# Optimization experiments

Measured on AMD Instinct MI355X. Metric: run time of the kernel, lower is better.

## Reference

```python
import jax, jax.numpy as jnp
import numpy as np

BATCH = 8192
EMBED = 1024
NFEAT = 32768
TOPK = 64


def setup_inputs() -> dict:
    key = jax.random.key(0)
    k1, k2, k3 = jax.random.split(key, 3)
    embed = jax.random.normal(k1, (BATCH, EMBED), dtype=jnp.float32)
    # nn.Linear-style init scale
    enc_w = jax.random.normal(k2, (NFEAT, EMBED), dtype=jnp.float32) * (1.0 / np.sqrt(EMBED))
    enc_b = jnp.zeros((NFEAT,), dtype=jnp.float32)
    dec_table = jax.random.normal(k3, (NFEAT, EMBED), dtype=jnp.float32)
    return {"embed": embed, "enc_w": enc_w, "enc_b": enc_b, "dec_table": dec_table}


def reference(embed, enc_w, enc_b, dec_table):
    # Encoder: linear + sigmoid -> [B, NFEAT]
    project = jax.nn.sigmoid(jnp.einsum('be,fe->bf', embed, enc_w) + enc_b)
    # Top-k selection along feature dim
    weights, feats = jax.lax.top_k(project, TOPK)   # [B, K] each
    # Decoder: gather embeddings and weighted sum -> [B, EMBED]
    vecs = dec_table[feats]                          # [B, K, EMBED]
    return jnp.einsum('bk,bke->be', weights, vecs)
```

## Files before the change

kernel.cpp:

```cpp
#include <hip/hip_runtime.h>
#include <hip/hip_bf16.h>

#define BATCH 8192
#define EMBED 1024
#define NFEAT 32768
#define TOPK  64
#define NT    16

#define CAP  512
#define GCAP 768
#define AMB  128
#define EPS2 0.028f
#define TMUL 2.4f

typedef __attribute__((ext_vector_type(8))) short bf16x8;
typedef __attribute__((ext_vector_type(4))) float f32x4;
typedef unsigned long long u64;

__device__ __forceinline__ void gload_lds16(const void* g, void* l) {
  __builtin_amdgcn_global_load_lds(
      (const __attribute__((address_space(1))) unsigned int*)g,
      (__attribute__((address_space(3))) unsigned int*)l, 16, 0, 0);
}

__device__ __forceinline__ unsigned short f2bf(float f) {
  unsigned int u = __float_as_uint(f);
  u += 0x7fffu + ((u >> 16) & 1u);
  return (unsigned short)(u >> 16);
}
__device__ __forceinline__ float bf2f(unsigned short u) {
  return __uint_as_float(((unsigned int)u) << 16);
}

__global__ __launch_bounds__(256) void k_zero(int* __restrict__ p, int n) {
  int i = blockIdx.x * 256 + threadIdx.x;
  if (i < n) p[i] = 0;
}

__global__ __launch_bounds__(256) void k_cvt(const float* __restrict__ in,
                                             unsigned short* __restrict__ out, long n) {
  long i = ((long)blockIdx.x * blockDim.x + threadIdx.x) * 4;
  long stride = (long)gridDim.x * blockDim.x * 4;
  for (; i < n; i += stride) {
    f32x4 v = *(const f32x4*)(in + i);
    u64 pk = (u64)f2bf(v[0]) | ((u64)f2bf(v[1]) << 16) |
             ((u64)f2bf(v[2]) << 32) | ((u64)f2bf(v[3]) << 48);
    *(u64*)(out + i) = pk;
  }
}

__global__ __launch_bounds__(256) void k_norm(const float* __restrict__ embed,
                                              float* __restrict__ T0) {
  const int row = blockIdx.x * 4 + (threadIdx.x >> 6);
  const int lane = threadIdx.x & 63;
  const float* e = embed + (size_t)row * EMBED;
  float ss = 0.f;
  for (int j = lane * 4; j < EMBED; j += 256) {
    f32x4 v = *(const f32x4*)(e + j);
    ss += v[0]*v[0] + v[1]*v[1] + v[2]*v[2] + v[3]*v[3];
  }
  #pragma unroll
  for (int off = 32; off > 0; off >>= 1) ss += __shfl_down(ss, off);
  if (lane == 0) T0[row] = TMUL * sqrtf(ss) * (1.0f / 32.0f);
}

#define PHASE(BUF, MH, NH, STG)                                               \
  {                                                                           \
    if (NH == 0) {                                                            \
      _Pragma("unroll")                                                       \
      for (int mi = 0; mi < 4; ++mi) {                                        \
        const int ar = wr * 128 + MH * 64 + mi * 16 + l15;                    \
        a[mi][0] = *(const bf16x8*)&As[BUF][ar][k0];                          \
        a[mi][1] = *(const bf16x8*)&As[BUF][ar][k1];                          \
      }                                                                       \
    }                                                                         \
    if (MH == 0) {                                                            \
      _Pragma("unroll")                                                       \
      for (int ni = 0; ni < 2; ++ni) {                                        \
        const int br = wc * 64 + NH * 32 + ni * 16 + l15;                     \
        (NH ? b1 : b0)[ni][0] = *(const bf16x8*)&Bs[BUF][br][k0];             \
        (NH ? b1 : b0)[ni][1] = *(const bf16x8*)&Bs[BUF][br][k1];             \
      }                                                                       \
    }                                                                         \
    STG;                                                                      \
    asm volatile("s_waitcnt vmcnt(8)" ::: "memory");                          \
    __builtin_amdgcn_s_barrier();                                             \
    __builtin_amdgcn_s_setprio(1);                                            \
    _Pragma("unroll")                                                         \
    for (int mi = 0; mi < 4; ++mi) {                                          \
      _Pragma("unroll")                                                       \
      for (int ni = 0; ni < 2; ++ni) {                                        \
        acc[MH*4+mi][NH*2+ni] = __builtin_amdgcn_mfma_f32_16x16x32_bf16(      \
            a[mi][0], (NH ? b1 : b0)[ni][0], acc[MH*4+mi][NH*2+ni], 0, 0, 0); \
        acc[MH*4+mi][NH*2+ni] = __builtin_amdgcn_mfma_f32_16x16x32_bf16(      \
            a[mi][1], (NH ? b1 : b0)[ni][1], acc[MH*4+mi][NH*2+ni], 0, 0, 0); \
      }                                                                       \
    }                                                                         \
    __builtin_amdgcn_s_setprio(0);                                            \
    __builtin_amdgcn_s_barrier();                                             \
  }

__global__ __launch_bounds__(512, 2) void k_gemm(
    const unsigned short* __restrict__ A,
    const unsigned short* __restrict__ B,
    const float* __restrict__ bias,
    const float* __restrict__ T0,
    u64* __restrict__ gent,
    int* __restrict__ cntB)
{
  __shared__ unsigned short As[2][256][64];
  __shared__ unsigned short Bs[2][256][64];
  __shared__ float T0s[256];
  __shared__ float lval[GCAP];
  __shared__ int   lpak[GCAP];
  __shared__ int   lcnt;

  const int tid = threadIdx.x;
  const int w = tid >> 6, lane = tid & 63;
  const int l15 = lane & 15, l4 = lane >> 4;
  const int wr = w >> 2, wc = w & 3;

  const int id = blockIdx.y * gridDim.x + blockIdx.x;
  const int xcd = id & 7;
  const int idx = id >> 3;
  const int ntile = xcd * 16 + (idx & 15);
  const int mtile = idx >> 4;

  const unsigned short* Ag = A + (size_t)mtile * 256 * EMBED;
  const unsigned short* Bg = B + (size_t)ntile * 256 * EMBED;

  const int rr = tid >> 3;
  const int u3 = tid & 7;
  const int scol = (u3 ^ (rr & 7)) << 3;
  const size_t aoff = (size_t)rr * EMBED + scol;
  const int brr = ((rr >> 5) << 6) + (rr & 31);
  const size_t boff = (size_t)brr * EMBED + scol;
  const int wrow = w * 8;
  const int bdst = ((w >> 2) << 6) + ((w & 3) << 3);

  const int k0 = (l4 ^ (l15 & 7)) << 3;
  const int k1 = k0 ^ 32;

  auto SA = [&](int tt, int r0, int r1) {
    if (tt < NT) {
      const int bb = tt & 1;
      const size_t kt = (size_t)tt * 64;
      gload_lds16(Ag + (size_t)r0 * EMBED + kt + aoff, (void*)&As[bb][r0 + wrow][0]);
      gload_lds16(Ag + (size_t)r1 * EMBED + kt + aoff, (void*)&As[bb][r1 + wrow][0]);
    }
  };
  auto SB = [&](int tt, int sb) {
    if (tt < NT) {
      const int bb = tt & 1;
      const size_t kt = (size_t)tt * 64;
      gload_lds16(Bg + (size_t)sb * EMBED + kt + boff, (void*)&Bs[bb][sb + bdst][0]);
      gload_lds16(Bg + (size_t)(sb + 128) * EMBED + kt + boff,
                  (void*)&Bs[bb][sb + 128 + bdst][0]);
    }
  };

  f32x4 acc[8][4] = {};
  bf16x8 a[4][2], b0[2][2], b1[2][2];

  SA(0, 0, 128); SB(0, 0); SB(0, 32); SA(0, 64, 192); SA(1, 0, 128); SB(1, 0);
  asm volatile("s_waitcnt vmcnt(8)" ::: "memory");
  __builtin_amdgcn_s_barrier();

  for (int t = 0; t < NT; t += 2) {
    PHASE(0, 0, 0, SB(t + 1, 32));
    PHASE(0, 0, 1, SA(t + 1, 64, 192));
    PHASE(0, 1, 0, SA(t + 2, 0, 128));
    PHASE(0, 1, 1, SB(t + 2, 0));
    PHASE(1, 0, 0, SB(t + 2, 32));
    PHASE(1, 0, 1, SA(t + 2, 64, 192));
    PHASE(1, 1, 0, SA(t + 3, 0, 128));
    PHASE(1, 1, 1, SB(t + 3, 0));
  }

  if (tid == 0) lcnt = 0;
  if (tid < 256) T0s[tid] = T0[mtile * 256 + tid];
  __syncthreads();

  const int col = l15, rg = l4 * 4;
  #pragma unroll
  for (int N = 0; N < 4; ++N) {
    const int n = ntile * 256 + wc * 64 + N * 16 + col;
    const float bv = bias[n];
    #pragma unroll
    for (int M = 0; M < 8; ++M) {
      const int rbase = wr * 128 + M * 16 + rg;
      #pragma unroll
      for (int j = 0; j < 4; ++j) {
        const float s = acc[M][N][j] + bv;
        const int rl = rbase + j;
        if (s >= T0s[rl]) {
          const int p = atomicAdd(&lcnt, 1);
          if (p < GCAP) { lval[p] = s; lpak[p] = (rl << 16) | n; }
        }
      }
    }
  }
  __syncthreads();
  const int bslot = mtile * 128 + ntile;
  int c = lcnt; if (c > GCAP) c = GCAP;
  if (tid == 0) cntB[bslot] = c;
  u64* gb = gent + (size_t)bslot * GCAP;
  for (int e = tid; e < c; e += 512)
    gb[e] = ((u64)(unsigned)lpak[e] << 32) | (u64)__float_as_uint(lval[e]);
}

__global__ __launch_bounds__(512) void k_compact(
    const u64* __restrict__ gent, const int* __restrict__ cntB,
    float* __restrict__ cval, int* __restrict__ cidx, int* __restrict__ ccnt)
{
  const int mtile = blockIdx.x >> 3, g = blockIdx.x & 7;
  const int tid = threadIdx.x;
  __shared__ int cnt[256], base[256], cur[256];
  __shared__ int bc[16];
  if (tid < 256) { cnt[tid] = 0; cur[tid] = 0; }
  if (tid < 16) bc[tid] = cntB[mtile * 128 + g * 16 + tid];
  __syncthreads();
  for (int i = 0; i < 16; ++i) {
    const int c = bc[i];
    const u64* bp = gent + (size_t)(mtile * 128 + g * 16 + i) * GCAP;
    for (int e = tid; e < c; e += 512)
      atomicAdd(&cnt[(int)(bp[e] >> 48)], 1);
  }
  __syncthreads();
  if (tid < 256) base[tid] = atomicAdd(&ccnt[mtile * 256 + tid], cnt[tid]);
  __syncthreads();
  for (int i = 0; i < 16; ++i) {
    const int c = bc[i];
    const u64* bp = gent + (size_t)(mtile * 128 + g * 16 + i) * GCAP;
    for (int e = tid; e < c; e += 512) {
      const u64 u = bp[e];
      const int pack = (int)(u >> 32);
      const int rl = pack >> 16, n = pack & 0xFFFF;
      const int p = base[rl] + atomicAdd(&cur[rl], 1);
      if (p < CAP) {
        const size_t row = (size_t)mtile * 256 + rl;
        cval[row * CAP + p] = __uint_as_float((unsigned)u);
        cidx[row * CAP + p] = n;
      }
    }
  }
}

__global__ __launch_bounds__(256) void k_sel(
    const float* __restrict__ cval_g, const int* __restrict__ cidx_g,
    const int* __restrict__ ccnt, const float* __restrict__ T0,
    int* __restrict__ def_idx, float* __restrict__ def_val,
    int* __restrict__ amb_idx, int* __restrict__ def_cnt, int* __restrict__ amb_cnt)
{
  const int row = blockIdx.x;
  const int tid = threadIdx.x;
  int n = ccnt[row]; if (n > CAP) n = CAP;
  __shared__ float v[CAP];
  __shared__ int ix[CAP];
  __shared__ int dcnt, acnt;
  if (tid == 0) { dcnt = 0; acnt = 0; }
  for (int e = tid; e < CAP; e += 256) {
    if (e < n) { v[e] = cval_g[(size_t)row * CAP + e]; ix[e] = cidx_g[(size_t)row * CAP + e]; }
    else       { v[e] = -3.0e38f; ix[e] = -1; }
  }
  __syncthreads();

  for (int k = 2; k <= CAP; k <<= 1) {
    for (int j = k >> 1; j > 0; j >>= 1) {
      const int i = ((tid & ~(j - 1)) << 1) | (tid & (j - 1));
      const int p = i | j;
      const bool desc = ((i & k) == 0);
      const float av = v[i], bv = v[p];
      if (desc ? (av < bv) : (av > bv)) {
        v[i] = bv; v[p] = av;
        int t2 = ix[i]; ix[i] = ix[p]; ix[p] = t2;
      }
      __syncthreads();
    }
  }

  const float T = T0[row];
  for (int e = tid; e < CAP; e += 256) {
    if (e >= n) continue;
    const float myv = v[e];
    const float tU = myv - EPS2, tL = myv + EPS2;
    int lo = 0, hi = CAP;
    while (lo < hi) { int m = (lo + hi) >> 1; if (v[m] >= tU) lo = m + 1; else hi = m; }
    const int U = lo;
    lo = 0; hi = CAP;
    while (lo < hi) { int m = (lo + hi) >> 1; if (v[m] > tL) lo = m + 1; else hi = m; }
    const int L = lo;

    if (U <= TOPK && tU >= T) {
      int p = atomicAdd(&dcnt, 1);
      if (p < TOPK) {
        def_idx[(size_t)row * TOPK + p] = ix[e];
        def_val[(size_t)row * TOPK + p] = myv;
      }
    } else if (L < TOPK) {
      int p = atomicAdd(&acnt, 1);
      if (p < AMB) amb_idx[(size_t)row * AMB + p] = ix[e];
    }
  }
  __syncthreads();
  if (tid == 0) {
    def_cnt[row] = dcnt > TOPK ? TOPK : dcnt;
    amb_cnt[row] = acnt > AMB ? AMB : acnt;
  }
}

__global__ __launch_bounds__(256) void k_final(
    const float* __restrict__ embed, const float* __restrict__ encw,
    const float* __restrict__ bias,
    const int* __restrict__ def_idx, const float* __restrict__ def_val,
    const int* __restrict__ amb_idx, const int* __restrict__ def_cnt,
    const int* __restrict__ amb_cnt,
    int* __restrict__ feats, float* __restrict__ weights)
{
  const int row = blockIdx.x;
  const int tid = threadIdx.x;
  const int d = def_cnt[row];
  const int a = amb_cnt[row];

  for (int i = tid; i < TOPK; i += 256) {
    feats[(size_t)row * TOPK + i] = 0;
    weights[(size_t)row * TOPK + i] = 0.0f;
  }
  __syncthreads();

  for (int i = tid; i < d; i += 256) {
    float v = def_val[(size_t)row * TOPK + i];
    feats[(size_t)row * TOPK + i] = def_idx[(size_t)row * TOPK + i];
    weights[(size_t)row * TOPK + i] = 1.0f / (1.0f + expf(-v));
  }
  if (d >= TOPK) return;

  __shared__ float e[EMBED];
  __shared__ double sc[AMB];
  __shared__ int si[AMB];
  for (int i = tid; i < EMBED; i += 256) e[i] = embed[(size_t)row * EMBED + i];
  __syncthreads();

  const int wv = tid >> 6, lane = tid & 63;
  for (int c = wv; c < a; c += 4) {
    const int f = amb_idx[(size_t)row * AMB + c];
    const float* wrp = encw + (size_t)f * EMBED;
    double p = 0.0;
    for (int j = lane; j < EMBED; j += 64) p += (double)e[j] * (double)wrp[j];
    #pragma unroll
    for (int off = 32; off > 0; off >>= 1) p += __shfl_down(p, off);
    if (lane == 0) { sc[c] = p + (double)bias[f]; si[c] = f; }
  }
  __syncthreads();

  const int need = TOPK - d;
  if (tid < a) {
    const double v = sc[tid];
    int r = 0;
    for (int j = 0; j < a; j++) {
      double u = sc[j];
      if (u > v || (u == v && j < tid)) r++;
    }
    if (r < need) {
      feats[(size_t)row * TOPK + d + r] = si[tid];
      weights[(size_t)row * TOPK + d + r] = (float)(1.0 / (1.0 + exp(-v)));
    }
  }
}

__global__ __launch_bounds__(128) void k_decode(
    const unsigned short* __restrict__ dec, const int* __restrict__ feats,
    const float* __restrict__ weights, float* __restrict__ out)
{
  const int row = blockIdx.x;
  const int tid = threadIdx.x;
  __shared__ float wv[TOPK];
  __shared__ int fv[TOPK];
  if (tid < TOPK) {
    wv[tid] = weights[(size_t)row * TOPK + tid];
    int f = feats[(size_t)row * TOPK + tid];
    fv[tid] = ((unsigned)f < (unsigned)NFEAT) ? f : 0;
  }
  __syncthreads();
  float acc[8] = {0.f, 0.f, 0.f, 0.f, 0.f, 0.f, 0.f, 0.f};
  #pragma unroll 4
  for (int k = 0; k < TOPK; k++) {
    const bf16x8 v = *(const bf16x8*)(dec + (size_t)fv[k] * EMBED + tid * 8);
    const float w = wv[k];
    #pragma unroll
    for (int j = 0; j < 8; j++) acc[j] += w * bf2f((unsigned short)v[j]);
  }
  f32x4 o0 = {acc[0], acc[1], acc[2], acc[3]};
  f32x4 o1 = {acc[4], acc[5], acc[6], acc[7]};
  *(f32x4*)(out + (size_t)row * EMBED + tid * 8)     = o0;
  *(f32x4*)(out + (size_t)row * EMBED + tid * 8 + 4) = o1;
}

__global__ __launch_bounds__(256) void k_decode_f32(
    const float* __restrict__ dec, const int* __restrict__ feats,
    const float* __restrict__ weights, float* __restrict__ out)
{
  const int row = blockIdx.x;
  const int tid = threadIdx.x;
  __shared__ float wv[TOPK];
  __shared__ int fv[TOPK];
  if (tid < TOPK) {
    wv[tid] = weights[(size_t)row * TOPK + tid];
    int f = feats[(size_t)row * TOPK + tid];
    fv[tid] = ((unsigned)f < (unsigned)NFEAT) ? f : 0;
  }
  __syncthreads();
  f32x4 acc = {0.f, 0.f, 0.f, 0.f};
  #pragma unroll 4
  for (int k = 0; k < TOPK; k++) {
    const f32x4 v = *(const f32x4*)(dec + (size_t)fv[k] * EMBED + tid * 4);
    const float w = wv[k];
    acc[0] += w * v[0]; acc[1] += w * v[1]; acc[2] += w * v[2]; acc[3] += w * v[3];
  }
  *(f32x4*)(out + (size_t)row * EMBED + tid * 4) = acc;
}

extern "C" void kernel_launch(void* const* d_in, const int* in_sizes, int n_in,
                              void* d_out, int out_size, void* d_ws, size_t ws_size,
                              hipStream_t stream) {
  const float* embed = (const float*)d_in[0];
  const float* enc_w = (const float*)d_in[1];
  const float* enc_b = (const float*)d_in[2];
  const float* dec   = (const float*)d_in[3];
  float* out = (float*)d_out;

  char* ws = (char*)d_ws;
  size_t off = 0;
  auto alloc = [&](size_t b) {
    void* p = ws + off;
    off = (off + b + 255) & ~(size_t)255;
    return p;
  };
  unsigned short* embed_bf = (unsigned short*)alloc((size_t)BATCH * EMBED * 2);
  unsigned short* encw_bf  = (unsigned short*)alloc((size_t)NFEAT * EMBED * 2);
  u64*   gent    = (u64*)  alloc((size_t)4096 * GCAP * 8);
  int*   cntB    = (int*)  alloc((size_t)4096 * 4);
  int*   ccnt    = (int*)  alloc((size_t)BATCH * 4);
  float* T0      = (float*)alloc((size_t)BATCH * 4);
  int*   def_idx = (int*)  alloc((size_t)BATCH * TOPK * 4);
  float* def_val = (float*)alloc((size_t)BATCH * TOPK * 4);
  int*   amb_idx = (int*)  alloc((size_t)BATCH * AMB * 4);
  int*   def_cnt = (int*)  alloc((size_t)BATCH * 4);
  int*   amb_cnt = (int*)  alloc((size_t)BATCH * 4);
  int*   feats   = (int*)  alloc((size_t)BATCH * TOPK * 4);
  float* weights = (float*)alloc((size_t)BATCH * TOPK * 4);

  float* cval = (float*)encw_bf;
  int*   cidx = (int*)((char*)encw_bf + (size_t)BATCH * CAP * 4);

  unsigned short* dec_bf = nullptr;
  if (off + (size_t)NFEAT * EMBED * 2 <= ws_size)
    dec_bf = (unsigned short*)alloc((size_t)NFEAT * EMBED * 2);

  k_zero<<<(BATCH + 255) / 256, 256, 0, stream>>>(ccnt, BATCH);
  k_cvt<<<1024, 256, 0, stream>>>(embed, embed_bf, (long)BATCH * EMBED);
  k_cvt<<<2048, 256, 0, stream>>>(enc_w, encw_bf, (long)NFEAT * EMBED);
  if (dec_bf)
    k_cvt<<<2048, 256, 0, stream>>>(dec, dec_bf, (long)NFEAT * EMBED);
  k_norm<<<BATCH / 4, 256, 0, stream>>>(embed, T0);

  k_gemm<<<dim3(NFEAT / 256, BATCH / 256), 512, 0, stream>>>(
      embed_bf, encw_bf, enc_b, T0, gent, cntB);
  k_compact<<<256, 512, 0, stream>>>(gent, cntB, cval, cidx, ccnt);

  k_sel<<<BATCH, 256, 0, stream>>>(cval, cidx, ccnt, T0,
                                   def_idx, def_val, amb_idx, def_cnt, amb_cnt);
  k_final<<<BATCH, 256, 0, stream>>>(embed, enc_w, enc_b, def_idx, def_val,
                                     amb_idx, def_cnt, amb_cnt, feats, weights);
  if (dec_bf)
    k_decode<<<BATCH, 128, 0, stream>>>(dec_bf, feats, weights, out);
  else
    k_decode_f32<<<BATCH, 256, 0, stream>>>(dec, feats, weights, out);
}
```

Before: 1.176 ms.

## Merge GEMM phases into four per K-pair and interleave A loads with MFMAs

The bf16 MFMA main loop goes from eight phases (M-half by N-half) to four phases per pair of K tiles. Each phase now covers the full N width, issues two global-to-LDS stages before a single barrier, and loads A fragments inside the MFMA loop instead of beforehand. Sched_barriers pin the ordering and the vmcnt wait count is adjusted to match. The aim is to halve the number of barriers and cut register pressure from the A fragment arrays. In exchange, each global prefetch now runs ahead of its use by less distance, and LDS reads are no longer hidden behind the barrier.

```diff
diff --git a/kernel.cpp b/kernel.cpp
--- a/kernel.cpp
+++ b/kernel.cpp
@@ -64,40 +64,40 @@
   if (lane == 0) T0[row] = TMUL * sqrtf(ss) * (1.0f / 32.0f);
 }
 
-#define PHASE(BUF, MH, NH, STG)                                               \
+#define PHASE(BUF, MH, STG)                                                   \
   {                                                                           \
-    if (NH == 0) {                                                            \
-      _Pragma("unroll")                                                       \
-      for (int mi = 0; mi < 4; ++mi) {                                        \
-        const int ar = wr * 128 + MH * 64 + mi * 16 + l15;                    \
-        a[mi][0] = *(const bf16x8*)&As[BUF][ar][k0];                          \
-        a[mi][1] = *(const bf16x8*)&As[BUF][ar][k1];                          \
-      }                                                                       \
-    }                                                                         \
+    STG;                                                                      \
+    asm volatile("s_waitcnt vmcnt(4)" ::: "memory");                          \
+    __builtin_amdgcn_s_barrier();                                             \
+    __builtin_amdgcn_sched_barrier(0);                                        \
+    __builtin_amdgcn_s_setprio(1);                                            \
     if (MH == 0) {                                                            \
       _Pragma("unroll")                                                       \
       for (int ni = 0; ni < 2; ++ni) {                                        \
-        const int br = wc * 64 + NH * 32 + ni * 16 + l15;                     \
-        (NH ? b1 : b0)[ni][0] = *(const bf16x8*)&Bs[BUF][br][k0];             \
-        (NH ? b1 : b0)[ni][1] = *(const bf16x8*)&Bs[BUF][br][k1];             \
+        const int br0 = wc * 64 + ni * 16 + l15;                              \
+        b0[ni][0] = *(const bf16x8*)&Bs[BUF][br0][k0];                        \
+        b0[ni][1] = *(const bf16x8*)&Bs[BUF][br0][k1];                        \
+        b1[ni][0] = *(const bf16x8*)&Bs[BUF][br0 + 32][k0];                   \
+        b1[ni][1] = *(const bf16x8*)&Bs[BUF][br0 + 32][k1];                   \
       }                                                                       \
     }                                                                         \
-    STG;                                                                      \
-    asm volatile("s_waitcnt vmcnt(8)" ::: "memory");                          \
-    __builtin_amdgcn_s_barrier();                                             \
-    __builtin_amdgcn_s_setprio(1);                                            \
     _Pragma("unroll")                                                         \
     for (int mi = 0; mi < 4; ++mi) {                                          \
-      _Pragma("unroll")                                                       \
-      for (int ni = 0; ni < 2; ++ni) {                                        \
-        acc[MH*4+mi][NH*2+ni] = __builtin_amdgcn_mfma_f32_16x16x32_bf16(      \
-            a[mi][0], (NH ? b1 : b0)[ni][0], acc[MH*4+mi][NH*2+ni], 0, 0, 0); \
-        acc[MH*4+mi][NH*2+ni] = __builtin_amdgcn_mfma_f32_16x16x32_bf16(      \
-            a[mi][1], (NH ? b1 : b0)[ni][1], acc[MH*4+mi][NH*2+ni], 0, 0, 0); \
-      }                                                                       \
+      const int ar = wr * 128 + (MH) * 64 + mi * 16 + l15;                    \
+      const bf16x8 a0 = *(const bf16x8*)&As[BUF][ar][k0];                     \
+      const bf16x8 a1 = *(const bf16x8*)&As[BUF][ar][k1];                     \
+      acc[(MH)*4+mi][0] = __builtin_amdgcn_mfma_f32_16x16x32_bf16(a0, b0[0][0], acc[(MH)*4+mi][0], 0, 0, 0); \
+      acc[(MH)*4+mi][0] = __builtin_amdgcn_mfma_f32_16x16x32_bf16(a1, b0[0][1], acc[(MH)*4+mi][0], 0, 0, 0); \
+      acc[(MH)*4+mi][1] = __builtin_amdgcn_mfma_f32_16x16x32_bf16(a0, b0[1][0], acc[(MH)*4+mi][1], 0, 0, 0); \
+      acc[(MH)*4+mi][1] = __builtin_amdgcn_mfma_f32_16x16x32_bf16(a1, b0[1][1], acc[(MH)*4+mi][1], 0, 0, 0); \
+      acc[(MH)*4+mi][2] = __builtin_amdgcn_mfma_f32_16x16x32_bf16(a0, b1[0][0], acc[(MH)*4+mi][2], 0, 0, 0); \
+      acc[(MH)*4+mi][2] = __builtin_amdgcn_mfma_f32_16x16x32_bf16(a1, b1[0][1], acc[(MH)*4+mi][2], 0, 0, 0); \
+      acc[(MH)*4+mi][3] = __builtin_amdgcn_mfma_f32_16x16x32_bf16(a0, b1[1][0], acc[(MH)*4+mi][3], 0, 0, 0); \
+      acc[(MH)*4+mi][3] = __builtin_amdgcn_mfma_f32_16x16x32_bf16(a1, b1[1][1], acc[(MH)*4+mi][3], 0, 0, 0); \
     }                                                                         \
     __builtin_amdgcn_s_setprio(0);                                            \
     __builtin_amdgcn_s_barrier();                                             \
+    __builtin_amdgcn_sched_barrier(0);                                        \
   }
 
 __global__ __launch_bounds__(512, 2) void k_gemm(
@@ -160,21 +160,18 @@
   };
 
   f32x4 acc[8][4] = {};
-  bf16x8 a[4][2], b0[2][2], b1[2][2];
-
-  SA(0, 0, 128); SB(0, 0); SB(0, 32); SA(0, 64, 192); SA(1, 0, 128); SB(1, 0);
-  asm volatile("s_waitcnt vmcnt(8)" ::: "memory");
+  bf16x8 b0[2][2], b1[2][2];
+
+  SA(0, 0, 128); SB(0, 0); SA(0, 64, 192); SB(0, 32); SA(1, 0, 128); SB(1, 0);
+  asm volatile("s_waitcnt vmcnt(4)" ::: "memory");
   __builtin_amdgcn_s_barrier();
+  __builtin_amdgcn_sched_barrier(0);
 
   for (int t = 0; t < NT; t += 2) {
-    PHASE(0, 0, 0, SB(t + 1, 32));
-    PHASE(0, 0, 1, SA(t + 1, 64, 192));
-    PHASE(0, 1, 0, SA(t + 2, 0, 128));
-    PHASE(0, 1, 1, SB(t + 2, 0));
-    PHASE(1, 0, 0, SB(t + 2, 32));
-    PHASE(1, 0, 1, SA(t + 2, 64, 192));
-    PHASE(1, 1, 0, SA(t + 3, 0, 128));
-    PHASE(1, 1, 1, SB(t + 3, 0));
+    PHASE(0, 0, { SA(t + 1, 64, 192); SB(t + 1, 32); });
+    PHASE(0, 1, { SA(t + 2, 0, 128);  SB(t + 2, 0);  });
+    PHASE(1, 0, { SA(t + 2, 64, 192); SB(t + 2, 32); });
+    PHASE(1, 1, { SA(t + 3, 0, 128);  SB(t + 3, 0);  });
   }
 
   if (tid == 0) lcnt = 0;
```

Result: slower. 1.301 ms (+10.6%).
